# Kernel tuning notes

Measured on AMD Instinct MI355X. Metric: run time of the kernel, lower is better.

The kernel has to match this reference:

```python
import jax, jax.numpy as jnp
import numpy as np

D = 1024

def setup_inputs() -> dict:
    key = jax.random.key(0)
    ks = jax.random.split(key, 7)
    s = D ** -0.5
    return {
        "x": jax.random.normal(ks[0], (8, 2048, D), dtype=jnp.float32),
        "Wq": jax.random.normal(ks[1], (D, D), dtype=jnp.float32) * s,
        "bq": jax.random.normal(ks[2], (D,), dtype=jnp.float32) * 0.02,
        "Wk": jax.random.normal(ks[3], (D, D), dtype=jnp.float32) * s,
        "bk": jax.random.normal(ks[4], (D,), dtype=jnp.float32) * 0.02,
        "Wv": jax.random.normal(ks[5], (D, D), dtype=jnp.float32) * s,
        "bv": jax.random.normal(ks[6], (D,), dtype=jnp.float32) * 0.02,
    }

def reference(x, Wq, bq, Wk, bk, Wv, bv):
    # torch nn.Linear: y = x @ W.T + b; here W stored as (D_in, D_out) directly.
    scaling = jnp.asarray(D, x.dtype) ** -0.5
    q = (jnp.einsum('btd,de->bte', x, Wq) + bq) * scaling
    k = jnp.einsum('btd,de->bte', x, Wk) + bk
    v = jnp.einsum('btd,de->bte', x, Wv) + bv
    attn = jax.nn.softmax(jnp.einsum('bqd,bkd->bqk', q, k), axis=-1)
    return jnp.einsum('bqk,bkd->bqd', attn, v)
```

## Files before the change

kernel.cpp:

```cpp
#include <hip/hip_runtime.h>

typedef unsigned short u16;
typedef __attribute__((ext_vector_type(8))) short short8;
typedef __attribute__((ext_vector_type(4))) float f32x4;
typedef __attribute__((ext_vector_type(4))) float f4;
typedef __attribute__((ext_vector_type(4))) unsigned short u16x4;

#define AS3 __attribute__((address_space(3)))
#define AS1 __attribute__((address_space(1)))

static __device__ __forceinline__ u16 f2b(float f) {
  unsigned int u = __builtin_bit_cast(unsigned int, f);
  u += 0x7FFFu + ((u >> 16) & 1u);
  return (u16)(u >> 16);
}

__global__ __launch_bounds__(256) void k_prep(const float* __restrict__ x,
                                              const float* __restrict__ Wq,
                                              const float* __restrict__ Wk,
                                              const float* __restrict__ Wv,
                                              const float* __restrict__ bq,
                                              const float* __restrict__ bk,
                                              const float* __restrict__ bv,
                                              u16* __restrict__ xb,
                                              u16* __restrict__ Wt,
                                              float* __restrict__ bcat,
                                              float* __restrict__ rsum) {
  __shared__ float t[32][33];
  int bid = blockIdx.x, tid = threadIdx.x;
  if (bid < 2048) {
    const int n4 = 8 * 2048 * 1024 / 4;
    int i = bid * 256 + tid;
    const int stride = 2048 * 256;
#pragma unroll 2
    for (; i < n4; i += stride) {
      f4 v = ((const f4*)x)[i];
      u16x4 o = { f2b(v[0]), f2b(v[1]), f2b(v[2]), f2b(v[3]) };
      ((u16x4*)xb)[i] = o;
    }
  } else if (bid < 5120) {
    int wi = bid - 2048;
    int z = wi >> 10;
    int r2 = wi & 1023;
    int kb = (r2 >> 5) * 32, nb = (r2 & 31) * 32;
    const float* W = z == 0 ? Wq : (z == 1 ? Wk : Wv);
    float scale = z == 0 ? 0.03125f : 1.0f;
    int tx = tid & 31, ty = tid >> 5;
#pragma unroll
    for (int i = 0; i < 4; i++) {
      int r = ty + i * 8;
      t[r][tx] = W[(long long)(kb + r) * 1024 + nb + tx];
    }
    __syncthreads();
#pragma unroll
    for (int i = 0; i < 4; i++) {
      int r = ty + i * 8;
      Wt[(long long)(z * 1024 + nb + r) * 1024 + kb + tx] = f2b(t[tx][r] * scale);
    }
  } else if (bid < 5132) {
    int i = (bid - 5120) * 256 + tid;
    if (i < 1024) bcat[i] = bq[i] * 0.03125f;
    else if (i < 2048) bcat[i] = bk[i - 1024];
    else if (i < 3072) bcat[i] = bv[i - 2048];
  } else {
    int i = (bid - 5132) * 256 + tid;
    if (i < 16384) rsum[i] = 0.0f;
  }
}


#define STAGE_U(MATBASE, GPTR, d_, ks_, kt_) do {                              \
    _Pragma("unroll")                                                          \
    for (int q_ = 0; q_ < 2; ++q_) {                                           \
      const u16* gp_ = (GPTR) + goff[q_] + (kt_) * 64 + (ks_) * 32;            \
      __builtin_amdgcn_global_load_lds((const AS1 void*)gp_,                   \
          (AS3 void*)(sm + (MATBASE) + ((d_) * 2 + (ks_)) * 16384 +            \
                      (wave * 2 + q_) * 1024), 16, 0, 0);                      \
    }                                                                          \
  } while (0)

#define PHASE(d_, ks_, mh_, STG, VM_) do {                                     \
    AS3 char* Asl_ = sm + ((d_) * 2 + (ks_)) * 16384;                          \
    AS3 char* Bsl_ = sm + 65536 + ((d_) * 2 + (ks_)) * 16384;                  \
    if ((mh_) == 0) {                                                          \
      _Pragma("unroll")                                                        \
      for (int nf_ = 0; nf_ < 4; ++nf_)                                        \
        bfr[nf_] = *(const AS3 short8*)(Bsl_ + boff[nf_]);                     \
    }                                                                          \
    _Pragma("unroll")                                                          \
    for (int mf_ = 0; mf_ < 4; ++mf_)                                          \
      afr[mf_] = *(const AS3 short8*)(Asl_ + aoff[mh_][mf_]);                  \
    STG;                                                                       \
    __builtin_amdgcn_s_barrier();                                              \
    __builtin_amdgcn_sched_barrier(0);                                         \
    __builtin_amdgcn_s_setprio(1);                                             \
    _Pragma("unroll")                                                          \
    for (int mf_ = 0; mf_ < 4; ++mf_)                                          \
      _Pragma("unroll")                                                        \
      for (int nf_ = 0; nf_ < 4; ++nf_)                                        \
        acc[(mh_) * 4 + mf_][nf_] = __builtin_amdgcn_mfma_f32_16x16x32_bf16(   \
            afr[mf_], bfr[nf_], acc[(mh_) * 4 + mf_][nf_], 0, 0, 0);           \
    __builtin_amdgcn_s_setprio(0);                                             \
    if (VM_) asm volatile("s_waitcnt vmcnt(4)" ::: "memory");                  \
    __builtin_amdgcn_s_barrier();                                              \
    __builtin_amdgcn_sched_barrier(0);                                         \
  } while (0)

template <int KD>
static __device__ __forceinline__ void gemm256(const u16* __restrict__ A,
                                               const u16* __restrict__ B,
                                               AS3 char* sm, f32x4 acc[8][4]) {
  constexpr int NT = KD / 64;
  const int tid = threadIdx.x, lane = tid & 63, wave = tid >> 6;
  const int wm = wave >> 2, wn = wave & 3;

  int goff[2];
#pragma unroll
  for (int q = 0; q < 2; ++q) {
    int P = (wave * 2 + q) * 1024 + lane * 16;
    int pr = P >> 6, pc = (P >> 4) & 3;
    int lc = pc ^ ((pr >> 1) & 3);
    goff[q] = pr * KD + lc * 8;
  }
  int aoff[2][4], boff[4];
#pragma unroll
  for (int mh = 0; mh < 2; ++mh)
#pragma unroll
    for (int mf = 0; mf < 4; ++mf) {
      int r = wm * 128 + mh * 64 + mf * 16 + (lane & 15);
      aoff[mh][mf] = r * 64 + ((((lane >> 4) ^ ((r >> 1) & 3))) << 4);
    }
#pragma unroll
  for (int nf = 0; nf < 4; ++nf) {
    int r = wn * 64 + nf * 16 + (lane & 15);
    boff[nf] = r * 64 + ((((lane >> 4) ^ ((r >> 1) & 3))) << 4);
  }

  short8 afr[4], bfr[4];

  STAGE_U(0, A, 0, 0, 0);
  STAGE_U(65536, B, 0, 0, 0);
  STAGE_U(0, A, 0, 1, 0);
  STAGE_U(65536, B, 0, 1, 0);
  STAGE_U(0, A, 1, 0, 1);
  STAGE_U(65536, B, 1, 0, 1);
  asm volatile("s_waitcnt vmcnt(4)" ::: "memory");
  __builtin_amdgcn_s_barrier();
  __builtin_amdgcn_sched_barrier(0);

  for (int i = 0; i < NT / 2; ++i) {
    int t1 = 2 * i + 1;
    int t2 = 2 * i + 2 < NT ? 2 * i + 2 : 0;
    int t3 = 2 * i + 3 < NT ? 2 * i + 3 : 1;
    PHASE(0, 0, 0, STAGE_U(0, A, 1, 1, t1), 0);
    PHASE(0, 0, 1, STAGE_U(65536, B, 1, 1, t1), 0);
    PHASE(0, 1, 0, STAGE_U(0, A, 0, 0, t2), 0);
    PHASE(0, 1, 1, STAGE_U(65536, B, 0, 0, t2), 1);
    PHASE(1, 0, 0, STAGE_U(0, A, 0, 1, t2), 0);
    PHASE(1, 0, 1, STAGE_U(65536, B, 0, 1, t2), 0);
    PHASE(1, 1, 0, STAGE_U(0, A, 1, 0, t3), 0);
    PHASE(1, 1, 1, STAGE_U(65536, B, 1, 0, t3), 1);
  }
  asm volatile("s_waitcnt vmcnt(0)" ::: "memory");
  __builtin_amdgcn_s_barrier();
}

__global__ __launch_bounds__(512, 2) void k_qkv256(const u16* __restrict__ xb,
                                                   const u16* __restrict__ Wt,
                                                   const float* __restrict__ bcat,
                                                   u16* __restrict__ Qb, u16* __restrict__ Kb,
                                                   u16* __restrict__ Vt) {
  extern __shared__ char smem_raw[];
  AS3 char* sm = (AS3 char*)smem_raw;
  int nx = gridDim.x;
  int id = blockIdx.y * nx + blockIdx.x;
  int qq = (nx * gridDim.y) >> 3;
  int nid = (id & 7) * qq + (id >> 3);
  int bx = nid % nx, by = nid / nx;
  const u16* A = xb + (long long)by * 256 * 1024;
  const u16* B = Wt + (long long)bx * 256 * 1024;
  f32x4 acc[8][4] = {};
  gemm256<1024>(A, B, sm, acc);
  int lane = threadIdx.x & 63, wave = threadIdx.x >> 6;
  int wm = wave >> 2, wn = wave & 3;
  int which = bx >> 2;
  if (which < 2) {
    u16* out = which == 0 ? Qb : Kb;
#pragma unroll
    for (int mf = 0; mf < 8; ++mf)
#pragma unroll
      for (int nf = 0; nf < 4; ++nf) {
        int colg = bx * 256 + wn * 64 + nf * 16 + (lane & 15);
        float bia = bcat[colg];
        int d = colg & 1023;
#pragma unroll
        for (int r = 0; r < 4; ++r) {
          int row = by * 256 + wm * 128 + mf * 16 + ((lane >> 4) << 2) + r;
          out[(long long)row * 1024 + d] = f2b(acc[mf][nf][r] + bia);
        }
      }
  } else {
    int b = (by * 256) >> 11;
    u16* vt = Vt + (long long)b * 1024 * 2048;
    int t0 = ((by * 256) & 2047) + wm * 128 + ((lane >> 4) << 2);
#pragma unroll
    for (int mf = 0; mf < 8; ++mf)
#pragma unroll
      for (int nf = 0; nf < 4; ++nf) {
        int colg = bx * 256 + wn * 64 + nf * 16 + (lane & 15);
        float bia = bcat[colg];
        int d = colg & 1023;
        u16x4 o = { f2b(acc[mf][nf][0] + bia), f2b(acc[mf][nf][1] + bia),
                    f2b(acc[mf][nf][2] + bia), f2b(acc[mf][nf][3] + bia) };
        *(u16x4*)&vt[(long long)d * 2048 + t0 + mf * 16] = o;
      }
  }
}

__global__ __launch_bounds__(512, 2) void k_qk256(const u16* __restrict__ Qb,
                                                  const u16* __restrict__ Kb,
                                                  u16* __restrict__ P, float* __restrict__ rsum,
                                                  int bbase, long long pStride) {
  extern __shared__ char smem_raw[];
  AS3 char* sm = (AS3 char*)smem_raw;
  int b = bbase + blockIdx.z;
  int nx = gridDim.x;
  int id = blockIdx.y * nx + blockIdx.x;
  int qq = (nx * gridDim.y) >> 3;
  int nid = (id & 7) * qq + (id >> 3);
  int bx = nid % nx, by = nid / nx;
  const u16* A = Qb + (long long)b * 2048 * 1024 + (long long)by * 256 * 1024;
  const u16* B = Kb + (long long)b * 2048 * 1024 + (long long)bx * 256 * 1024;
  f32x4 acc[8][4] = {};
  gemm256<1024>(A, B, sm, acc);
  u16* Pb = P + (long long)blockIdx.z * pStride;
  float* rs = rsum + (long long)b * 2048;
  int lane = threadIdx.x & 63, wave = threadIdx.x >> 6;
  int wm = wave >> 2, wn = wave & 3;
#pragma unroll
  for (int mf = 0; mf < 8; ++mf)
#pragma unroll
    for (int r = 0; r < 4; ++r) {
      int row = by * 256 + wm * 128 + mf * 16 + ((lane >> 4) << 2) + r;
      float s = 0.0f;
#pragma unroll
      for (int nf = 0; nf < 4; ++nf) {
        float e = __expf(acc[mf][nf][r]);
        Pb[(long long)row * 2048 + bx * 256 + wn * 64 + nf * 16 + (lane & 15)] = f2b(e);
        s += e;
      }
      s += __shfl_xor(s, 1);
      s += __shfl_xor(s, 2);
      s += __shfl_xor(s, 4);
      s += __shfl_xor(s, 8);
      if ((lane & 15) == 0) atomicAdd(&rs[row], s);
    }
}

__global__ __launch_bounds__(512, 2) void k_pv256(const u16* __restrict__ P,
                                                  const u16* __restrict__ Vt,
                                                  const float* __restrict__ rsum,
                                                  float* __restrict__ out,
                                                  int bbase, long long pStride) {
  extern __shared__ char smem_raw[];
  AS3 char* sm = (AS3 char*)smem_raw;
  int b = bbase + blockIdx.z;
  int nx = gridDim.x;
  int id = blockIdx.y * nx + blockIdx.x;
  int qq = (nx * gridDim.y) >> 3;
  int nid = (id & 7) * qq + (id >> 3);
  int bx = nid % nx, by = nid / nx;
  const u16* A = P + (long long)blockIdx.z * pStride + (long long)by * 256 * 2048;
  const u16* B = Vt + (long long)b * 1024 * 2048 + (long long)bx * 256 * 2048;
  f32x4 acc[8][4] = {};
  gemm256<2048>(A, B, sm, acc);
  float* ob = out + (long long)b * 2048 * 1024;
  const float* rs = rsum + (long long)b * 2048;
  int lane = threadIdx.x & 63, wave = threadIdx.x >> 6;
  int wm = wave >> 2, wn = wave & 3;
#pragma unroll
  for (int mf = 0; mf < 8; ++mf)
#pragma unroll
    for (int r = 0; r < 4; ++r) {
      int row = by * 256 + wm * 128 + mf * 16 + ((lane >> 4) << 2) + r;
      float inv = 1.0f / rs[row];
#pragma unroll
      for (int nf = 0; nf < 4; ++nf) {
        ob[(long long)row * 1024 + bx * 256 + wn * 64 + nf * 16 + (lane & 15)] =
            acc[mf][nf][r] * inv;
      }
    }
}

extern "C" void kernel_launch(void* const* d_in, const int* in_sizes, int n_in,
                              void* d_out, int out_size, void* d_ws, size_t ws_size,
                              hipStream_t stream) {
  const float* x = (const float*)d_in[0];
  const float* Wq = (const float*)d_in[1];
  const float* bq = (const float*)d_in[2];
  const float* Wk = (const float*)d_in[3];
  const float* bk = (const float*)d_in[4];
  const float* Wv = (const float*)d_in[5];
  const float* bv = (const float*)d_in[6];
  float* out = (float*)d_out;
  char* ws = (char*)d_ws;

  const long long B = 8, T = 2048, D = 1024, BT = B * T;

  size_t off = 0;
  auto alloc = [&](size_t bytes) {
    size_t r = off;
    off += (bytes + 255) & ~(size_t)255;
    return r;
  };
  size_t oXB = alloc(BT * D * 2);
  size_t oWT = alloc((size_t)3072 * 1024 * 2);
  size_t oBC = alloc(3072 * 4);
  size_t oQ = alloc(BT * D * 2);
  size_t oK = alloc(BT * D * 2);
  size_t oVT = alloc(BT * D * 2);
  size_t oRS = alloc(BT * 4);
  size_t oP = off;
  bool batched = ws_size >= off + (size_t)B * T * T * 2;

  u16* xb = (u16*)(ws + oXB);
  u16* Wt = (u16*)(ws + oWT);
  float* bcat = (float*)(ws + oBC);
  u16* Qb = (u16*)(ws + oQ);
  u16* Kb = (u16*)(ws + oK);
  u16* Vt = (u16*)(ws + oVT);
  float* rsum = (float*)(ws + oRS);
  u16* P = (u16*)(ws + oP);

  (void)hipFuncSetAttribute((const void*)k_qkv256, hipFuncAttributeMaxDynamicSharedMemorySize, 131072);
  (void)hipFuncSetAttribute((const void*)k_qk256, hipFuncAttributeMaxDynamicSharedMemorySize, 131072);
  (void)hipFuncSetAttribute((const void*)k_pv256, hipFuncAttributeMaxDynamicSharedMemorySize, 131072);

  k_prep<<<dim3(5196), dim3(256), 0, stream>>>(x, Wq, Wk, Wv, bq, bk, bv, xb, Wt, bcat, rsum);
  k_qkv256<<<dim3(12, 64, 1), dim3(512), 131072, stream>>>(xb, Wt, bcat, Qb, Kb, Vt);

  if (batched) {
    k_qk256<<<dim3(8, 8, 8), dim3(512), 131072, stream>>>(Qb, Kb, P, rsum, 0, T * T);
    k_pv256<<<dim3(4, 8, 8), dim3(512), 131072, stream>>>(P, Vt, rsum, out, 0, T * T);
  } else {
    for (int b = 0; b < 8; b++) {
      k_qk256<<<dim3(8, 8, 1), dim3(512), 131072, stream>>>(Qb, Kb, P, rsum, b, 0);
      k_pv256<<<dim3(4, 8, 1), dim3(512), 131072, stream>>>(P, Vt, rsum, out, b, 0);
    }
  }
}
```

Before: 388.4 us.

## Alias P buffer over dead staging buffers and remap block tile order

Reorders the workspace so the P score buffer starts at offset zero, overlapping the bf16 x and transposed-weight buffers, which are dead once the QKV projection finishes. If the workspace cannot hold all 8 batches it falls back to groups of 4 batches instead of one batch per launch. The block index remapping in the QK and PV kernels is replaced with an explicit 2x4 (or 2x2) tile grouping aimed at better L2 locality for shared Q/K rows. This assumes the aliasing is safe given stream ordering, and the swizzle hardcodes grid dimensions.

```diff
diff --git a/kernel.cpp b/kernel.cpp
--- a/kernel.cpp
+++ b/kernel.cpp
@@ -67,7 +67,6 @@
     if (i < 16384) rsum[i] = 0.0f;
   }
 }
-
 
 #define STAGE_U(MATBASE, GPTR, d_, ks_, kt_) do {                              \
     _Pragma("unroll")                                                          \
@@ -224,11 +223,10 @@
   extern __shared__ char smem_raw[];
   AS3 char* sm = (AS3 char*)smem_raw;
   int b = bbase + blockIdx.z;
-  int nx = gridDim.x;
-  int id = blockIdx.y * nx + blockIdx.x;
-  int qq = (nx * gridDim.y) >> 3;
-  int nid = (id & 7) * qq + (id >> 3);
-  int bx = nid % nx, by = nid / nx;
+  int i = blockIdx.y * 8 + blockIdx.x;
+  int xk = i & 7, j = i >> 3;
+  int by = ((xk >> 1) << 1) + (j >> 2);
+  int bx = ((xk & 1) << 2) + (j & 3);
   const u16* A = Qb + (long long)b * 2048 * 1024 + (long long)by * 256 * 1024;
   const u16* B = Kb + (long long)b * 2048 * 1024 + (long long)bx * 256 * 1024;
   f32x4 acc[8][4] = {};
@@ -265,11 +263,10 @@
   extern __shared__ char smem_raw[];
   AS3 char* sm = (AS3 char*)smem_raw;
   int b = bbase + blockIdx.z;
-  int nx = gridDim.x;
-  int id = blockIdx.y * nx + blockIdx.x;
-  int qq = (nx * gridDim.y) >> 3;
-  int nid = (id & 7) * qq + (id >> 3);
-  int bx = nid % nx, by = nid / nx;
+  int i = blockIdx.y * 4 + blockIdx.x;
+  int xk = i & 7, j = i >> 3;
+  int by = ((xk >> 1) << 1) + (j >> 1);
+  int bx = ((xk & 1) << 1) + (j & 1);
   const u16* A = P + (long long)blockIdx.z * pStride + (long long)by * 256 * 2048;
   const u16* B = Vt + (long long)b * 1024 * 2048 + (long long)bx * 256 * 2048;
   f32x4 acc[8][4] = {};
@@ -307,30 +304,39 @@
 
   const long long B = 8, T = 2048, D = 1024, BT = B * T;
 
-  size_t off = 0;
+  const size_t xbB = (size_t)BT * D * 2;
+  const size_t wtB = (size_t)3072 * 1024 * 2;
+  const size_t r0min = ((xbB + 255) & ~(size_t)255) + ((wtB + 255) & ~(size_t)255);
+  const size_t pSlice = (size_t)T * T * 2;
+
+  int g = 8;
+  size_t r0 = (size_t)8 * pSlice;
+  {
+    auto al = [](size_t v) { return (v + 255) & ~(size_t)255; };
+    size_t tail = al(3072 * 4) + 3 * al(xbB) + al(BT * 4);
+    if (ws_size < r0 + tail) { g = 4; r0 = r0min > (size_t)4 * pSlice ? r0min : (size_t)4 * pSlice; }
+  }
+
+  size_t off = r0;
   auto alloc = [&](size_t bytes) {
     size_t r = off;
     off += (bytes + 255) & ~(size_t)255;
     return r;
   };
-  size_t oXB = alloc(BT * D * 2);
-  size_t oWT = alloc((size_t)3072 * 1024 * 2);
   size_t oBC = alloc(3072 * 4);
-  size_t oQ = alloc(BT * D * 2);
-  size_t oK = alloc(BT * D * 2);
-  size_t oVT = alloc(BT * D * 2);
+  size_t oQ = alloc(xbB);
+  size_t oK = alloc(xbB);
+  size_t oVT = alloc(xbB);
   size_t oRS = alloc(BT * 4);
-  size_t oP = off;
-  bool batched = ws_size >= off + (size_t)B * T * T * 2;
-
-  u16* xb = (u16*)(ws + oXB);
-  u16* Wt = (u16*)(ws + oWT);
+
+  u16* xb = (u16*)(ws + 0);
+  u16* Wt = (u16*)(ws + ((xbB + 255) & ~(size_t)255));
+  u16* P = (u16*)(ws + 0);
   float* bcat = (float*)(ws + oBC);
   u16* Qb = (u16*)(ws + oQ);
   u16* Kb = (u16*)(ws + oK);
   u16* Vt = (u16*)(ws + oVT);
   float* rsum = (float*)(ws + oRS);
-  u16* P = (u16*)(ws + oP);
 
   (void)hipFuncSetAttribute((const void*)k_qkv256, hipFuncAttributeMaxDynamicSharedMemorySize, 131072);
   (void)hipFuncSetAttribute((const void*)k_qk256, hipFuncAttributeMaxDynamicSharedMemorySize, 131072);
@@ -339,13 +345,8 @@
   k_prep<<<dim3(5196), dim3(256), 0, stream>>>(x, Wq, Wk, Wv, bq, bk, bv, xb, Wt, bcat, rsum);
   k_qkv256<<<dim3(12, 64, 1), dim3(512), 131072, stream>>>(xb, Wt, bcat, Qb, Kb, Vt);
 
-  if (batched) {
-    k_qk256<<<dim3(8, 8, 8), dim3(512), 131072, stream>>>(Qb, Kb, P, rsum, 0, T * T);
-    k_pv256<<<dim3(4, 8, 8), dim3(512), 131072, stream>>>(P, Vt, rsum, out, 0, T * T);
-  } else {
-    for (int b = 0; b < 8; b++) {
-      k_qk256<<<dim3(8, 8, 1), dim3(512), 131072, stream>>>(Qb, Kb, P, rsum, b, 0);
-      k_pv256<<<dim3(4, 8, 1), dim3(512), 131072, stream>>>(P, Vt, rsum, out, b, 0);
-    }
-  }
-}
+  for (int c = 0; c < 8 / g; ++c) {
+    k_qk256<<<dim3(8, 8, g), dim3(512), 131072, stream>>>(Qb, Kb, P, rsum, c * g, pSlice);
+    k_pv256<<<dim3(4, 8, g), dim3(512), 131072, stream>>>(P, Vt, rsum, out, c * g, pSlice);
+  }
+}
```

After: 382.9 us. About the same (-1.4%).
